# Kernel optimization log

Measured on AMD Instinct MI355X. Metric: run time of the kernel, lower is better.

The kernel has to match this reference:

```python
import jax, jax.numpy as jnp
import numpy as np

LN_EPS = 1e-5  # torch.nn.LayerNorm default


def setup_inputs() -> dict:
    key = jax.random.key(0)
    k1, k2 = jax.random.split(key)
    C = 64
    x = jax.random.normal(k1, (1, C, 64, 96, 96), dtype=jnp.float32)
    ln_gamma = jnp.ones((C,), jnp.float32)
    ln_beta = jnp.zeros((C,), jnp.float32)
    # Conv3d(C, 3C, 1, groups=C) -> per-channel scalar weight [3C] and bias [3C]
    conv_w = jax.random.normal(k2, (3 * C,), dtype=jnp.float32) * 0.02
    conv_b = jnp.zeros((3 * C,), jnp.float32)
    return {"x": x, "ln_gamma": ln_gamma, "ln_beta": ln_beta,
            "conv_w": conv_w, "conv_b": conv_b}


def reference(x, ln_gamma, ln_beta, conv_w, conv_b):
    B, C, D, H, W = x.shape
    N = D * H * W
    xf = x.reshape(B, C, N)  # [B, C, N]

    # LayerNorm over the channel dim (module permutes channels last)
    mean = jnp.mean(xf, axis=1, keepdims=True)
    var = jnp.mean(jnp.square(xf - mean), axis=1, keepdims=True)
    y = (xf - mean) * jax.lax.rsqrt(var + LN_EPS)
    y = y * ln_gamma[None, :, None] + ln_beta[None, :, None]

    # grouped 1x1x1 conv: output channel o reads input channel o // 3
    idx = jnp.arange(3 * C) // 3
    y3 = y[:, idx, :] * conv_w[None, :, None] + conv_b[None, :, None]  # [B, 3C, N]
    q, k, v = jnp.split(y3, 3, axis=1)  # each [B, C, N]

    # channel (cross-covariance) attention: logits [B, C, C]
    logits = jnp.einsum('bcn,bkn->bck', q, k) * (C ** -0.5)
    attn = jax.nn.softmax(logits, axis=-1)  # max-subtraction built in
    out = jnp.einsum('bck,bkn->bcn', attn, v).reshape(B, C, D, H, W)
    return x + out
```

## Files before the change

### kernel.cpp

```cpp
#include <hip/hip_runtime.h>

#define NPOS 589824
#define LN_EPS 1e-5f

typedef _Float16 half8 __attribute__((ext_vector_type(8)));
typedef _Float16 half2_t __attribute__((ext_vector_type(2)));
typedef float f32x4 __attribute__((ext_vector_type(4)));
typedef float f32x2 __attribute__((ext_vector_type(2)));

static __device__ __forceinline__ half2_t pk16(float a, float b) {
    return __builtin_bit_cast(half2_t, __builtin_amdgcn_cvt_pkrtz(a, b));
}

#define K1_BLOCKS 1152
#define YSTR 520


__global__ __launch_bounds__(256, 2) void csa_k1(
    const float* __restrict__ x, const float* __restrict__ lng,
    const float* __restrict__ lnb, float* __restrict__ partials)
{
    __shared__ __align__(16) _Float16 Y[45][YSTR];
    const int tid = threadIdx.x;
    const int lane = tid & 63;
    const int wv = tid >> 6;

    for (int i = tid; i < YSTR; i += 256) {
        Y[43][i] = (_Float16)1.0f;
        Y[44][i] = (_Float16)0.0f;
    }

    const int n0 = (blockIdx.x * 256 + tid) * 2;
    f32x2 xv[64];
    f32x2 s = {0.f, 0.f}, sq = s;
    #pragma unroll
    for (int c = 0; c < 64; ++c) {
        f32x2 v = *(const f32x2*)(x + (size_t)c * NPOS + n0);
        xv[c] = v; s += v; sq += v * v;
    }
    const f32x2 mu = s * (1.f/64.f);
    const f32x2 var = sq * (1.f/64.f) - mu * mu;
    const float rin0 = rsqrtf(fmaxf(var[0], 0.f) + LN_EPS);
    const float rin1 = rsqrtf(fmaxf(var[1], 0.f) + LN_EPS);
    #pragma unroll
    for (int c = 0; c < 43; ++c) {
        const float g = lng[c], b = lnb[c];
        const float y0 = fmaf((xv[c][0] - mu[0]) * rin0, g, b);
        const float y1 = fmaf((xv[c][1] - mu[1]) * rin1, g, b);
        *(half2_t*)&Y[c][tid * 2] = pk16(y0, y1);
    }
    __syncthreads();

    f32x4 acc00 = {0.f,0.f,0.f,0.f}, acc01 = acc00, acc10 = acc00, acc11 = acc00;
    const int row = lane & 15;
    const int sub = (lane >> 4) & 3;
    const int kbase = wv * 128 + sub * 8;
    const int r16 = row + 16;
    const int ra1 = (r16 < 22) ? r16 : ((r16 == 22) ? 43 : 44);
    const int rb1 = (r16 < 22) ? (r16 + 21) : ((r16 == 22) ? 43 : 44);
    #pragma unroll
    for (int s2 = 0; s2 < 4; ++s2) {
        const int kk = kbase + s2 * 32;
        half8 a0 = *(const half8*)&Y[row][kk];
        half8 a1 = *(const half8*)&Y[ra1][kk];
        half8 b0 = *(const half8*)&Y[row + 21][kk];
        half8 b1 = *(const half8*)&Y[rb1][kk];
        acc00 = __builtin_amdgcn_mfma_f32_16x16x32_f16(a0, b0, acc00, 0, 0, 0);
        acc01 = __builtin_amdgcn_mfma_f32_16x16x32_f16(a0, b1, acc01, 0, 0, 0);
        acc10 = __builtin_amdgcn_mfma_f32_16x16x32_f16(a1, b0, acc10, 0, 0, 0);
        acc11 = __builtin_amdgcn_mfma_f32_16x16x32_f16(a1, b1, acc11, 0, 0, 0);
    }
    __syncthreads();

    float* G32 = (float*)&Y[0][0];
    for (int e = tid; e < 1024; e += 256) G32[e] = 0.f;
    __syncthreads();
    const int r0 = (lane >> 4) * 4, c0 = lane & 15;
    #pragma unroll
    for (int r = 0; r < 4; ++r) {
        atomicAdd(&G32[(r0 + r) * 32 + c0],            acc00[r]);
        atomicAdd(&G32[(r0 + r) * 32 + 16 + c0],       acc01[r]);
        atomicAdd(&G32[(16 + r0 + r) * 32 + c0],       acc10[r]);
        atomicAdd(&G32[(16 + r0 + r) * 32 + 16 + c0],  acc11[r]);
    }
    __syncthreads();
    for (int e = tid; e < 576; e += 256) {
        const int r = e / 24, c = e % 24;
        partials[(size_t)blockIdx.x * 576 + e] = G32[r * 32 + c];
    }
}

__global__ __launch_bounds__(256) void csa_k2(const float* __restrict__ partials,
                                              float* __restrict__ gfin)
{
    const int tid = threadIdx.x;
    const int e = blockIdx.x * 16 + (tid >> 4);
    const int g = tid & 15;
    float s = 0.f;
    for (int b = g; b < K1_BLOCKS; b += 16)
        s += partials[(size_t)b * 576 + e];
    s += __shfl_down(s, 8, 16);
    s += __shfl_down(s, 4, 16);
    s += __shfl_down(s, 2, 16);
    s += __shfl_down(s, 1, 16);
    if (g == 0) gfin[e] = s;
}

__global__ void csa_k3(const float* __restrict__ G, const float* __restrict__ cw,
                       const float* __restrict__ cb, float* __restrict__ M,
                       float* __restrict__ betaO)
{
    const int c = threadIdx.x;
    __shared__ float lg[64][65];
    const float wq = cw[c], bq = cb[c];
    const int a = c / 3;
    const float Sa = G[a * 24 + 22];
    float mx = -1e30f;
    #pragma unroll
    for (int k = 0; k < 64; ++k) {
        const float wk = cw[64 + k], bk = cb[64 + k];
        const int b = (64 + k) / 3 - 21;
        const float Gab = G[a * 24 + b];
        const float Sb  = G[22 * 24 + b];
        float lo = 0.125f * (wq * wk * Gab + wq * bk * Sa + bq * wk * Sb
                             + bq * bk * (float)NPOS);
        lg[c][k] = lo;
        mx = fmaxf(mx, lo);
    }
    float sum = 0.f;
    #pragma unroll
    for (int k = 0; k < 64; ++k) {
        float e = expf(lg[c][k] - mx);
        lg[c][k] = e; sum += e;
    }
    const float inv = 1.f / sum;
    float Ml[22];
    #pragma unroll
    for (int m = 0; m < 22; ++m) Ml[m] = 0.f;
    float bacc = 0.f;
    #pragma unroll
    for (int k = 0; k < 64; ++k) {
        const float attn = lg[c][k] * inv;
        const int mm = (128 + k) / 3 - 42;
        Ml[mm] = fmaf(attn, cw[128 + k], Ml[mm]);
        bacc   = fmaf(attn, cb[128 + k], bacc);
    }
    #pragma unroll
    for (int m = 0; m < 22; ++m) M[c * 22 + m] = Ml[m];
    betaO[c] = bacc;
}

__global__ __launch_bounds__(256, 2) void csa_k4(
    const float* __restrict__ x, const float* __restrict__ lng,
    const float* __restrict__ lnb, const float* __restrict__ M,
    const float* __restrict__ betaO, float* __restrict__ out)
{
    const int n0 = (blockIdx.x * 256 + threadIdx.x) * 2;
    f32x2 xv[64];
    f32x2 s = {0.f, 0.f}, sq = s;
    #pragma unroll
    for (int c = 0; c < 64; ++c) {
        f32x2 v = *(const f32x2*)(x + (size_t)c * NPOS + n0);
        xv[c] = v; s += v; sq += v * v;
    }
    const f32x2 mu = s * (1.f/64.f);
    const f32x2 var = sq * (1.f/64.f) - mu * mu;
    const float rin0 = rsqrtf(fmaxf(var[0], 0.f) + LN_EPS);
    const float rin1 = rsqrtf(fmaxf(var[1], 0.f) + LN_EPS);
    f32x2 y[22];
    #pragma unroll
    for (int m = 0; m < 22; ++m) {
        const float g = lng[42 + m], b = lnb[42 + m];
        y[m][0] = fmaf((xv[42 + m][0] - mu[0]) * rin0, g, b);
        y[m][1] = fmaf((xv[42 + m][1] - mu[1]) * rin1, g, b);
    }
    #pragma unroll
    for (int c = 0; c < 64; ++c) {
        const float bb = betaO[c];
        f32x2 a = {bb, bb};
        #pragma unroll
        for (int m = 0; m < 22; ++m) {
            const float w = M[c * 22 + m];
            a[0] = fmaf(w, y[m][0], a[0]);
            a[1] = fmaf(w, y[m][1], a[1]);
        }
        f32x2 o = xv[c] + a;
        __builtin_nontemporal_store(o, (f32x2*)(out + (size_t)c * NPOS + n0));
    }
}

extern "C" void kernel_launch(void* const* d_in, const int* in_sizes, int n_in,
                              void* d_out, int out_size, void* d_ws, size_t ws_size,
                              hipStream_t stream) {
    const float* x   = (const float*)d_in[0];
    const float* lng = (const float*)d_in[1];
    const float* lnb = (const float*)d_in[2];
    const float* cw  = (const float*)d_in[3];
    const float* cb  = (const float*)d_in[4];
    float* out = (float*)d_out;

    float* wsf = (float*)d_ws;
    float* Gf  = wsf;
    float* Mf  = wsf + 1024;
    float* Bf  = wsf + 1024 + 64 * 22;
    float* Pf  = wsf + 4096;

    hipLaunchKernelGGL(csa_k1, dim3(K1_BLOCKS), dim3(256), 0, stream,
                       x, lng, lnb, Pf);
    hipLaunchKernelGGL(csa_k2, dim3(36), dim3(256), 0, stream, Pf, Gf);
    hipLaunchKernelGGL(csa_k3, dim3(1), dim3(64), 0, stream, Gf, cw, cb, Mf, Bf);
    hipLaunchKernelGGL(csa_k4, dim3(NPOS / 512), dim3(256), 0, stream,
                       x, lng, lnb, Mf, Bf, out);
}
```

Measured before the change: 141.8 us.

## Split LayerNorm statistics into a separate kernel ahead of the Gram pass

A new kernel computes the per-position LayerNorm mean and inverse std over all 64 channels with float4 loads and writes them to workspace. The Gram kernel then reads those stats and loads only the 43 channels it needs, so it no longer holds 64 channels in registers, and its launch bound rises to 3 blocks per CU. The aim is to cut register pressure and raise occupancy in the Gram kernel. The cost is an extra full pass over x plus a stats write and read, which adds substantial memory traffic and one more launch.

Result: slower. 167.4 us (+18.1%).

```diff
diff --git a/kernel.cpp b/kernel.cpp
--- a/kernel.cpp
+++ b/kernel.cpp
@@ -12,13 +12,39 @@
     return __builtin_bit_cast(half2_t, __builtin_amdgcn_cvt_pkrtz(a, b));
 }
 
-#define K1_BLOCKS 1152
+#define KB_BLOCKS 1152
 #define YSTR 520
 
 
-__global__ __launch_bounds__(256, 2) void csa_k1(
+__global__ __launch_bounds__(256) void csa_stats(
+    const float* __restrict__ x, float* __restrict__ stats)
+{
+    const int g = blockIdx.x * 256 + threadIdx.x;
+    const f32x4* __restrict__ x4 = (const f32x4*)x;
+    f32x4 s = {0.f,0.f,0.f,0.f}, sq = s;
+    #pragma unroll
+    for (int c = 0; c < 64; ++c) {
+        f32x4 v = x4[(size_t)c * (NPOS/4) + g];
+        s += v;
+        sq += v * v;
+    }
+    const f32x4 mu = s * (1.f/64.f);
+    const f32x4 var = sq * (1.f/64.f) - mu * mu;
+    f32x4 o0, o1;
+    o0[0] = mu[0]; o0[2] = mu[1]; o1[0] = mu[2]; o1[2] = mu[3];
+    o0[1] = rsqrtf(fmaxf(var[0], 0.f) + LN_EPS);
+    o0[3] = rsqrtf(fmaxf(var[1], 0.f) + LN_EPS);
+    o1[1] = rsqrtf(fmaxf(var[2], 0.f) + LN_EPS);
+    o1[3] = rsqrtf(fmaxf(var[3], 0.f) + LN_EPS);
+    f32x4* st4 = (f32x4*)stats;
+    st4[2*g]     = o0;
+    st4[2*g + 1] = o1;
+}
+
+__global__ __launch_bounds__(256, 3) void csa_gram(
     const float* __restrict__ x, const float* __restrict__ lng,
-    const float* __restrict__ lnb, float* __restrict__ partials)
+    const float* __restrict__ lnb, const float* __restrict__ stats,
+    float* __restrict__ partials)
 {
     __shared__ __align__(16) _Float16 Y[45][YSTR];
     const int tid = threadIdx.x;
@@ -30,23 +56,16 @@
         Y[44][i] = (_Float16)0.0f;
     }
 
-    const int n0 = (blockIdx.x * 256 + tid) * 2;
-    f32x2 xv[64];
-    f32x2 s = {0.f, 0.f}, sq = s;
-    #pragma unroll
-    for (int c = 0; c < 64; ++c) {
+    const int t = blockIdx.x * 256 + tid;
+    const f32x4 st = ((const f32x4*)stats)[t];
+    const float mu0 = st[0], rin0 = st[1], mu1 = st[2], rin1 = st[3];
+    const int n0 = t * 2;
+    #pragma unroll
+    for (int c = 0; c < 43; ++c) {
         f32x2 v = *(const f32x2*)(x + (size_t)c * NPOS + n0);
-        xv[c] = v; s += v; sq += v * v;
-    }
-    const f32x2 mu = s * (1.f/64.f);
-    const f32x2 var = sq * (1.f/64.f) - mu * mu;
-    const float rin0 = rsqrtf(fmaxf(var[0], 0.f) + LN_EPS);
-    const float rin1 = rsqrtf(fmaxf(var[1], 0.f) + LN_EPS);
-    #pragma unroll
-    for (int c = 0; c < 43; ++c) {
         const float g = lng[c], b = lnb[c];
-        const float y0 = fmaf((xv[c][0] - mu[0]) * rin0, g, b);
-        const float y1 = fmaf((xv[c][1] - mu[1]) * rin1, g, b);
+        const float y0 = fmaf((v[0] - mu0) * rin0, g, b);
+        const float y1 = fmaf((v[1] - mu1) * rin1, g, b);
         *(half2_t*)&Y[c][tid * 2] = pk16(y0, y1);
     }
     __syncthreads();
@@ -97,7 +116,7 @@
     const int e = blockIdx.x * 16 + (tid >> 4);
     const int g = tid & 15;
     float s = 0.f;
-    for (int b = g; b < K1_BLOCKS; b += 16)
+    for (int b = g; b < KB_BLOCKS; b += 16)
         s += partials[(size_t)b * 576 + e];
     s += __shfl_down(s, 8, 16);
     s += __shfl_down(s, 4, 16);
@@ -199,14 +218,17 @@
     const float* cb  = (const float*)d_in[4];
     float* out = (float*)d_out;
 
-    float* wsf = (float*)d_ws;
-    float* Gf  = wsf;
-    float* Mf  = wsf + 1024;
-    float* Bf  = wsf + 1024 + 64 * 22;
-    float* Pf  = wsf + 4096;
-
-    hipLaunchKernelGGL(csa_k1, dim3(K1_BLOCKS), dim3(256), 0, stream,
-                       x, lng, lnb, Pf);
+    float* wsf   = (float*)d_ws;
+    float* Gf    = wsf;
+    float* Mf    = wsf + 1024;
+    float* Bf    = wsf + 1024 + 64 * 22;
+    float* stats = (float*)((char*)d_ws + 16384);
+    float* Pf    = (float*)((char*)d_ws + 16384 + (size_t)NPOS * 8);
+
+    hipLaunchKernelGGL(csa_stats, dim3(NPOS / 1024), dim3(256), 0, stream,
+                       x, stats);
+    hipLaunchKernelGGL(csa_gram, dim3(KB_BLOCKS), dim3(256), 0, stream,
+                       x, lng, lnb, stats, Pf);
     hipLaunchKernelGGL(csa_k2, dim3(36), dim3(256), 0, stream, Pf, Gf);
     hipLaunchKernelGGL(csa_k3, dim3(1), dim3(64), 0, stream, Gf, cw, cb, Mf, Bf);
     hipLaunchKernelGGL(csa_k4, dim3(NPOS / 512), dim3(256), 0, stream,
```

## Split LayerNorm stats across half-blocks and tile Gram kernel over position chunks

Applied to the files above, without the earlier changes.

The Gram-accumulation kernel stops having each thread hold all 64 channels for two positions. Each half of the block now loads 32 channels for one position, and the two halves combine their sums through shared memory. The kernel walks four 128-position chunks and issues one MFMA step per chunk. This cuts the register footprint and the shared Y tile so more waves fit (launch bound 4), at the cost of extra barriers per chunk and scalar rather than paired loads.

After: 151.3 us. 6.7% more time.

```diff
diff --git a/kernel.cpp b/kernel.cpp
--- a/kernel.cpp
+++ b/kernel.cpp
@@ -4,63 +4,68 @@
 #define LN_EPS 1e-5f
 
 typedef _Float16 half8 __attribute__((ext_vector_type(8)));
-typedef _Float16 half2_t __attribute__((ext_vector_type(2)));
 typedef float f32x4 __attribute__((ext_vector_type(4)));
 typedef float f32x2 __attribute__((ext_vector_type(2)));
 
-static __device__ __forceinline__ half2_t pk16(float a, float b) {
-    return __builtin_bit_cast(half2_t, __builtin_amdgcn_cvt_pkrtz(a, b));
-}
-
 #define K1_BLOCKS 1152
-#define YSTR 520
-
-
-__global__ __launch_bounds__(256, 2) void csa_k1(
+#define TILE 128
+#define CPB 4
+#define YSTR 136
+
+
+__global__ __launch_bounds__(256, 4) void csa_k1(
     const float* __restrict__ x, const float* __restrict__ lng,
     const float* __restrict__ lnb, float* __restrict__ partials)
 {
     __shared__ __align__(16) _Float16 Y[45][YSTR];
+    __shared__ float SS[256], QQ[256];
     const int tid = threadIdx.x;
     const int lane = tid & 63;
     const int wv = tid >> 6;
+    const int p127 = tid & 127;
+    const int c0 = (tid >> 7) * 32;
 
     for (int i = tid; i < YSTR; i += 256) {
         Y[43][i] = (_Float16)1.0f;
         Y[44][i] = (_Float16)0.0f;
     }
 
-    const int n0 = (blockIdx.x * 256 + tid) * 2;
-    f32x2 xv[64];
-    f32x2 s = {0.f, 0.f}, sq = s;
-    #pragma unroll
-    for (int c = 0; c < 64; ++c) {
-        f32x2 v = *(const f32x2*)(x + (size_t)c * NPOS + n0);
-        xv[c] = v; s += v; sq += v * v;
-    }
-    const f32x2 mu = s * (1.f/64.f);
-    const f32x2 var = sq * (1.f/64.f) - mu * mu;
-    const float rin0 = rsqrtf(fmaxf(var[0], 0.f) + LN_EPS);
-    const float rin1 = rsqrtf(fmaxf(var[1], 0.f) + LN_EPS);
-    #pragma unroll
-    for (int c = 0; c < 43; ++c) {
-        const float g = lng[c], b = lnb[c];
-        const float y0 = fmaf((xv[c][0] - mu[0]) * rin0, g, b);
-        const float y1 = fmaf((xv[c][1] - mu[1]) * rin1, g, b);
-        *(half2_t*)&Y[c][tid * 2] = pk16(y0, y1);
-    }
-    __syncthreads();
-
     f32x4 acc00 = {0.f,0.f,0.f,0.f}, acc01 = acc00, acc10 = acc00, acc11 = acc00;
     const int row = lane & 15;
     const int sub = (lane >> 4) & 3;
-    const int kbase = wv * 128 + sub * 8;
+    const int kk = wv * 32 + sub * 8;
     const int r16 = row + 16;
     const int ra1 = (r16 < 22) ? r16 : ((r16 == 22) ? 43 : 44);
     const int rb1 = (r16 < 22) ? (r16 + 21) : ((r16 == 22) ? 43 : 44);
-    #pragma unroll
-    for (int s2 = 0; s2 < 4; ++s2) {
-        const int kk = kbase + s2 * 32;
+    const int pos0 = blockIdx.x * (CPB * TILE);
+
+    for (int ck = 0; ck < CPB; ++ck) {
+        const int n = pos0 + ck * TILE + p127;
+        float xv[32];
+        #pragma unroll
+        for (int i = 0; i < 32; ++i)
+            xv[i] = x[(size_t)(c0 + i) * NPOS + n];
+        float s = 0.f, sq = 0.f;
+        #pragma unroll
+        for (int i = 0; i < 32; ++i) { s += xv[i]; sq = fmaf(xv[i], xv[i], sq); }
+        SS[tid] = s; QQ[tid] = sq;
+        __syncthreads();
+        const float st = SS[p127] + SS[p127 + 128];
+        const float qt = QQ[p127] + QQ[p127 + 128];
+        const float mu  = st * (1.f/64.f);
+        const float var = fmaf(-mu, mu, qt * (1.f/64.f));
+        const float rin = rsqrtf(fmaxf(var, 0.f) + LN_EPS);
+        if (c0 == 0) {
+            #pragma unroll
+            for (int i = 0; i < 32; ++i)
+                Y[i][p127] = (_Float16)fmaf((xv[i] - mu) * rin, lng[i], lnb[i]);
+        } else {
+            #pragma unroll
+            for (int i = 0; i < 11; ++i)
+                Y[32 + i][p127] =
+                    (_Float16)fmaf((xv[i] - mu) * rin, lng[32 + i], lnb[32 + i]);
+        }
+        __syncthreads();
         half8 a0 = *(const half8*)&Y[row][kk];
         half8 a1 = *(const half8*)&Y[ra1][kk];
         half8 b0 = *(const half8*)&Y[row + 21][kk];
@@ -69,19 +74,19 @@
         acc01 = __builtin_amdgcn_mfma_f32_16x16x32_f16(a0, b1, acc01, 0, 0, 0);
         acc10 = __builtin_amdgcn_mfma_f32_16x16x32_f16(a1, b0, acc10, 0, 0, 0);
         acc11 = __builtin_amdgcn_mfma_f32_16x16x32_f16(a1, b1, acc11, 0, 0, 0);
-    }
-    __syncthreads();
+        __syncthreads();
+    }
 
     float* G32 = (float*)&Y[0][0];
     for (int e = tid; e < 1024; e += 256) G32[e] = 0.f;
     __syncthreads();
-    const int r0 = (lane >> 4) * 4, c0 = lane & 15;
+    const int r0 = (lane >> 4) * 4, cc = lane & 15;
     #pragma unroll
     for (int r = 0; r < 4; ++r) {
-        atomicAdd(&G32[(r0 + r) * 32 + c0],            acc00[r]);
-        atomicAdd(&G32[(r0 + r) * 32 + 16 + c0],       acc01[r]);
-        atomicAdd(&G32[(16 + r0 + r) * 32 + c0],       acc10[r]);
-        atomicAdd(&G32[(16 + r0 + r) * 32 + 16 + c0],  acc11[r]);
+        atomicAdd(&G32[(r0 + r) * 32 + cc],            acc00[r]);
+        atomicAdd(&G32[(r0 + r) * 32 + 16 + cc],       acc01[r]);
+        atomicAdd(&G32[(16 + r0 + r) * 32 + cc],       acc10[r]);
+        atomicAdd(&G32[(16 + r0 + r) * 32 + 16 + cc],  acc11[r]);
     }
     __syncthreads();
     for (int e = tid; e < 576; e += 256) {
@@ -203,7 +208,7 @@
     float* Gf  = wsf;
     float* Mf  = wsf + 1024;
     float* Bf  = wsf + 1024 + 64 * 22;
-    float* Pf  = wsf + 4096;
+    float* Pf  = (float*)((char*)d_ws + 16384);
 
     hipLaunchKernelGGL(csa_k1, dim3(K1_BLOCKS), dim3(256), 0, stream,
                        x, lng, lnb, Pf);
```
